# Kernel optimization log

Hardware: AMD Instinct MI355X
Metric: run time of the kernel (lower is better)

## Reference

```python
import jax, jax.numpy as jnp
import numpy as np

B, T, D = 64, 8192, 128

def setup_inputs() -> dict:
    key = jax.random.key(0)
    ks = jax.random.split(key, 6)
    H_r = jax.random.normal(ks[0], (B, T, D), dtype=jnp.float32)
    mask_r = jax.random.randint(ks[1], (B, T), 0, 2, dtype=jnp.int32)
    h_tm1 = jax.random.normal(ks[2], (B, D), dtype=jnp.float32)
    # xavier-ish scaling for linear weights
    s = 1.0 / np.sqrt(D)
    V_w = jax.random.normal(ks[3], (D, D), dtype=jnp.float32) * s
    Wa_w = jax.random.normal(ks[4], (D, D), dtype=jnp.float32) * s
    V_b = jnp.zeros((D,), dtype=jnp.float32)
    Wa_b = jnp.zeros((D,), dtype=jnp.float32)
    v = jax.random.normal(ks[5], (D,), dtype=jnp.float32) * 0.05
    c = jnp.ones((1,), dtype=jnp.float32)
    return {"H_r": H_r, "mask_r": mask_r, "h_tm1": h_tm1, "V_w": V_w,
            "V_b": V_b, "Wa_w": Wa_w, "Wa_b": Wa_b, "v": v, "c": c}

def masked_softmax(x, m, axis=-1):
    x = jnp.clip(x, -15.0, 15.0)
    x = x * m
    e_x = jnp.exp(x - jnp.max(x, axis=axis, keepdims=True))
    e_x = e_x * m
    return e_x / (jnp.sum(e_x, axis=axis, keepdims=True) + 1e-6)

def reference(H_r, mask_r, h_tm1, V_w, V_b, Wa_w, Wa_b, v, c):
    m = mask_r.astype(jnp.float32)                      # [B,T]
    Fk = jnp.einsum('btd,od->bto', H_r, V_w) + V_b      # [B,T,D]
    Fk_prime = h_tm1 @ Wa_w.T + Wa_b                    # [B,D]
    Fk = jnp.tanh(Fk + Fk_prime[:, None, :])
    beta = Fk @ v + c                                   # [B,T]
    beta = masked_softmax(beta, m, axis=-1)
    z = jnp.einsum('bt,btd->bd', beta, H_r)             # [B,D]
    return (z, beta)
```

## Files before the change

### kernel.cpp

```cpp
#include <hip/hip_runtime.h>
#include <math.h>

#define BB 64
#define TT 8192
#define DD 128
#define RPT 64
#define NT 8
#define RPBLK (RPT * NT)
#define NBLK (BB * TT / RPBLK)
#define BPB (TT / RPBLK)

typedef float f32x4 __attribute__((ext_vector_type(4)));
typedef __bf16 bf16x8 __attribute__((ext_vector_type(8)));

__device__ __forceinline__ float fast_tanh(float x) {
    float t = __expf(2.f * x);
    return 1.f - 2.f * __builtin_amdgcn_rcpf(t + 1.f);
}

__device__ __forceinline__ bf16x8 cvt8(f32x4 a, f32x4 b) {
    bf16x8 r;
    r[0] = (__bf16)a[0]; r[1] = (__bf16)a[1]; r[2] = (__bf16)a[2]; r[3] = (__bf16)a[3];
    r[4] = (__bf16)b[0]; r[5] = (__bf16)b[1]; r[6] = (__bf16)b[2]; r[7] = (__bf16)b[3];
    return r;
}

__global__ __launch_bounds__(256) void convw_kernel(const float* __restrict__ Vw,
                                                    __bf16* __restrict__ Vw_bf) {
    const int i = blockIdx.x * 256 + threadIdx.x;
    const int r = i >> 7, cidx = i & 127;
    Vw_bf[r * DD + (cidx ^ ((r & 7) << 3))] = (__bf16)Vw[i];
}

__global__ __launch_bounds__(DD) void fkprime_kernel(
    const float* __restrict__ Waw, const float* __restrict__ Wab,
    const float* __restrict__ h_tm1, float* __restrict__ fkp) {
    const int b = blockIdx.x;
    const int o = threadIdx.x;
    const float* __restrict__ w = Waw + o * DD;
    const float* __restrict__ h = h_tm1 + b * DD;
    float a0 = 0.f, a1 = 0.f, a2 = 0.f, a3 = 0.f;
#pragma unroll
    for (int d = 0; d < DD; d += 4) {
        float4 w4 = *reinterpret_cast<const float4*>(w + d);
        a0 = fmaf(w4.x, h[d + 0], a0);
        a1 = fmaf(w4.y, h[d + 1], a1);
        a2 = fmaf(w4.z, h[d + 2], a2);
        a3 = fmaf(w4.w, h[d + 3], a3);
    }
    fkp[b * DD + o] = (a0 + a1) + (a2 + a3) + Wab[o];
}

__global__ __launch_bounds__(256, 2) void beta_z_kernel(
    const float* __restrict__ H, const __bf16* __restrict__ Vw_bf,
    const float* __restrict__ Vb, const float* __restrict__ fkp,
    const float* __restrict__ vvec, const float* __restrict__ cptr,
    const int* __restrict__ mask,
    float* __restrict__ eout,
    float* __restrict__ zpart) {
    const int tid  = threadIdx.x;
    const int wv   = tid >> 6;
    const int lane = tid & 63;
    const int cl   = lane & 15;
    const int kg   = lane >> 4;
    const int base_row = blockIdx.x * RPBLK;
    const int b    = base_row >> 13;

    __shared__ __align__(16) char s_vw[DD * DD * 2];
    __shared__ __align__(16) char s_h[RPT * DD * 4];
    __shared__ float s_z[4][DD];

    {
        const char* __restrict__ wg = (const char*)Vw_bf;
#pragma unroll
        for (int i = 0; i < 8; ++i) {
            __builtin_amdgcn_global_load_lds(
                (const void*)(wg + wv * 8192 + i * 1024 + lane * 16),
                (void*)(s_vw + wv * 8192 + i * 1024), 16, 0, 0);
        }
    }
    {
        const char* __restrict__ hb =
            (const char*)H + (size_t)(base_row + wv * 16) * 512;
#pragma unroll
        for (int i = 0; i < 8; ++i) {
            const int off  = i * 1024 + lane * 16;
            const int r16  = off >> 9;
            __builtin_amdgcn_global_load_lds(
                (const void*)(hb + (off ^ ((r16 & 7) << 4))),
                (void*)(s_h + wv * 8192 + i * 1024), 16, 0, 0);
        }
    }
    __syncthreads();

    const float cval = cptr[0];
    float biasv[8], vvv[8];
#pragma unroll
    for (int nt = 0; nt < 8; ++nt) {
        const int col = nt * 16 + cl;
        biasv[nt] = Vb[col] + fkp[b * DD + col];
        vvv[nt]   = vvec[col];
    }

    const int ra   = wv * 16 + cl;
    const int swzA = (cl & 7) << 4;
    f32x4 zlo[4], zhi[4];
#pragma unroll
    for (int kk = 0; kk < 4; ++kk) {
        zlo[kk] = (f32x4){0.f, 0.f, 0.f, 0.f};
        zhi[kk] = (f32x4){0.f, 0.f, 0.f, 0.f};
    }

    for (int t = 0; t < NT; ++t) {
        const int grow0 = base_row + t * RPT + wv * 16;
        const float mfl = (float)mask[grow0 + cl];

        f32x4 alo[4], ahi[4];
        bf16x8 af[4];
#pragma unroll
        for (int kk = 0; kk < 4; ++kk) {
            const int abyte = ra * 512 + kk * 128 + kg * 32;
            alo[kk] = *reinterpret_cast<const f32x4*>(s_h + ((abyte)      ^ swzA));
            ahi[kk] = *reinterpret_cast<const f32x4*>(s_h + ((abyte + 16) ^ swzA));
            af[kk]  = cvt8(alo[kk], ahi[kk]);
        }
        __builtin_amdgcn_sched_barrier(0);

        if (t + 1 < NT) {
            const char* __restrict__ hb =
                (const char*)H + (size_t)(grow0 + RPT) * 512;
#pragma unroll
            for (int i = 0; i < 8; ++i) {
                const int off = i * 1024 + lane * 16;
                const int r16 = off >> 9;
                __builtin_amdgcn_global_load_lds(
                    (const void*)(hb + (off ^ ((r16 & 7) << 4))),
                    (void*)(s_h + wv * 8192 + i * 1024), 16, 0, 0);
            }
        }

        f32x4 acc[8];
#pragma unroll
        for (int nt = 0; nt < 8; ++nt) acc[nt] = (f32x4){0.f, 0.f, 0.f, 0.f};
#pragma unroll
        for (int kk = 0; kk < 4; ++kk) {
#pragma unroll
            for (int nt = 0; nt < 8; ++nt) {
                const int rb    = nt * 16 + cl;
                const int bbyte = (rb * 256 + kk * 64 + kg * 16) ^ ((rb & 7) << 4);
                bf16x8 bfr = *reinterpret_cast<const bf16x8*>(s_vw + bbyte);
                acc[nt] = __builtin_amdgcn_mfma_f32_16x16x32_bf16(af[kk], bfr, acc[nt], 0, 0, 0);
            }
        }

        float part[4] = {0.f, 0.f, 0.f, 0.f};
#pragma unroll
        for (int nt = 0; nt < 8; ++nt) {
#pragma unroll
            for (int j = 0; j < 4; ++j)
                part[j] = fmaf(fast_tanh(acc[nt][j] + biasv[nt]), vvv[nt], part[j]);
        }
#pragma unroll
        for (int off = 1; off < 16; off <<= 1) {
#pragma unroll
            for (int j = 0; j < 4; ++j) part[j] += __shfl_xor(part[j], off);
        }
        float epj[4];
#pragma unroll
        for (int j = 0; j < 4; ++j) {
            const float mv = __shfl(mfl, kg * 4 + j);
            const float x  = fminf(fmaxf(cval + part[j], -15.f), 15.f);
            epj[j] = __expf(x * mv - 15.f) * mv;
        }
        if (cl == 0) {
#pragma unroll
            for (int j = 0; j < 4; ++j) eout[grow0 + kg * 4 + j] = epj[j];
        }

        float er0 = __shfl(epj[0], (cl >> 2) << 4);
        float er1 = __shfl(epj[1], (cl >> 2) << 4);
        float er2 = __shfl(epj[2], (cl >> 2) << 4);
        float er3 = __shfl(epj[3], (cl >> 2) << 4);
        const int sel = cl & 3;
        float e_cl = sel == 0 ? er0 : (sel == 1 ? er1 : (sel == 2 ? er2 : er3));
#pragma unroll
        for (int kk = 0; kk < 4; ++kk) {
#pragma unroll
            for (int j = 0; j < 4; ++j) {
                zlo[kk][j] = fmaf(e_cl, alo[kk][j], zlo[kk][j]);
                zhi[kk][j] = fmaf(e_cl, ahi[kk][j], zhi[kk][j]);
            }
        }

        if (t + 1 < NT) asm volatile("s_waitcnt vmcnt(0)" ::: "memory");
    }

#pragma unroll
    for (int off = 1; off < 16; off <<= 1) {
#pragma unroll
        for (int kk = 0; kk < 4; ++kk) {
#pragma unroll
            for (int j = 0; j < 4; ++j) {
                zlo[kk][j] += __shfl_xor(zlo[kk][j], off);
                zhi[kk][j] += __shfl_xor(zhi[kk][j], off);
            }
        }
    }
    if (cl == 0) {
#pragma unroll
        for (int kk = 0; kk < 4; ++kk) {
#pragma unroll
            for (int j = 0; j < 4; ++j) {
                s_z[wv][kk * 32 + kg * 8 + j]     = zlo[kk][j];
                s_z[wv][kk * 32 + kg * 8 + 4 + j] = zhi[kk][j];
            }
        }
    }
    __syncthreads();
    if (tid < DD) {
        zpart[(size_t)blockIdx.x * DD + tid] =
            (s_z[0][tid] + s_z[1][tid]) + (s_z[2][tid] + s_z[3][tid]);
    }
}

__global__ __launch_bounds__(256) void denom_kernel(
    float* __restrict__ eout, const int* __restrict__ mask,
    float* __restrict__ denom) {
    const int b = blockIdx.x, tid = threadIdx.x;
    float* __restrict__ e = eout + (size_t)b * TT;
    const int* __restrict__ mrow = mask + (size_t)b * TT;
    __shared__ float sE[256], sM[256];
    __shared__ int sA[256];

    float E = 0.f, M = 0.f;
    int any0 = 0;
    for (int t = tid; t < TT; t += 256) {
        float ep = e[t];
        E += ep;
        M = fmaxf(M, ep);
        any0 |= (mrow[t] == 0);
    }
    sE[tid] = E; sM[tid] = M; sA[tid] = any0;
    __syncthreads();
    for (int s = 128; s > 0; s >>= 1) {
        if (tid < s) {
            sE[tid] += sE[tid + s];
            sM[tid] = fmaxf(sM[tid], sM[tid + s]);
            sA[tid] |= sA[tid + s];
        }
        __syncthreads();
    }
    const float scale = sA[0] ? fmaxf(sM[0], 3.0590232e-7f ) : sM[0];
    const float dn = sE[0] + 1e-6f * scale;
    if (tid == 0) denom[b] = dn;
    const float inv = 1.f / dn;
    for (int t = tid; t < TT; t += 256) e[t] *= inv;
}

__global__ __launch_bounds__(256) void zfinal_kernel(
    const float* __restrict__ zpart, const float* __restrict__ denom,
    float* __restrict__ out_z) {
    const int idx = blockIdx.x * 256 + threadIdx.x;
    const int b = idx >> 7, d = idx & 127;
    const float* __restrict__ zp = zpart + (size_t)b * BPB * DD + d;
    float s = 0.f;
#pragma unroll
    for (int cc = 0; cc < BPB; ++cc) s += zp[cc * DD];
    out_z[idx] = s / denom[b];
}

extern "C" void kernel_launch(void* const* d_in, const int* in_sizes, int n_in,
                              void* d_out, int out_size, void* d_ws, size_t ws_size,
                              hipStream_t stream) {
    const float* H     = (const float*)d_in[0];
    const int*   mask  = (const int*)d_in[1];
    const float* h_tm1 = (const float*)d_in[2];
    const float* V_w   = (const float*)d_in[3];
    const float* V_b   = (const float*)d_in[4];
    const float* Wa_w  = (const float*)d_in[5];
    const float* Wa_b  = (const float*)d_in[6];
    const float* v     = (const float*)d_in[7];
    const float* c     = (const float*)d_in[8];

    float* out_z    = (float*)d_out;
    float* out_beta = (float*)d_out + BB * DD;

    float* ws     = (float*)d_ws;
    float* fkp    = ws;
    float* zpart  = fkp + BB * DD;
    float* denom  = zpart + NBLK * DD;
    __bf16* Vw_bf = (__bf16*)(denom + BB);

    convw_kernel<<<(DD * DD) / 256, 256, 0, stream>>>(V_w, Vw_bf);
    fkprime_kernel<<<BB, DD, 0, stream>>>(Wa_w, Wa_b, h_tm1, fkp);
    beta_z_kernel<<<NBLK, 256, 0, stream>>>(H, Vw_bf, V_b, fkp, v, c, mask,
                                            out_beta, zpart);
    denom_kernel<<<BB, 256, 0, stream>>>(out_beta, mask, denom);
    zfinal_kernel<<<(BB * DD) / 256, 256, 0, stream>>>(zpart, denom, out_z);
}
```

Baseline: 95.74 us.

## Stage H as bf16 in double-buffered LDS via registers, fuse auxiliary kernels

The main kernel now loads H tiles into registers, converts them to bf16, and writes them into a double-buffered LDS area, replacing direct global-to-LDS fp32 loads and per-iteration conversion. The z accumulation now uses the bf16 copy of H instead of fp32. Rows per block double, which halves the block count. The prep kernels and the denom/zfinal kernels are each fused into one kernel, cutting launches. This trades z precision (bf16 H) and adds a block-wide barrier every iteration plus register staging.

```diff
diff --git a/kernel.cpp b/kernel.cpp
--- a/kernel.cpp
+++ b/kernel.cpp
@@ -5,12 +5,13 @@
 #define TT 8192
 #define DD 128
 #define RPT 64
-#define NT 8
+#define NT 16
 #define RPBLK (RPT * NT)
 #define NBLK (BB * TT / RPBLK)
 #define BPB (TT / RPBLK)
 
 typedef float f32x4 __attribute__((ext_vector_type(4)));
+typedef __bf16 bf16x4 __attribute__((ext_vector_type(4)));
 typedef __bf16 bf16x8 __attribute__((ext_vector_type(8)));
 
 __device__ __forceinline__ float fast_tanh(float x) {
@@ -18,37 +19,32 @@
     return 1.f - 2.f * __builtin_amdgcn_rcpf(t + 1.f);
 }
 
-__device__ __forceinline__ bf16x8 cvt8(f32x4 a, f32x4 b) {
-    bf16x8 r;
-    r[0] = (__bf16)a[0]; r[1] = (__bf16)a[1]; r[2] = (__bf16)a[2]; r[3] = (__bf16)a[3];
-    r[4] = (__bf16)b[0]; r[5] = (__bf16)b[1]; r[6] = (__bf16)b[2]; r[7] = (__bf16)b[3];
-    return r;
-}
-
-__global__ __launch_bounds__(256) void convw_kernel(const float* __restrict__ Vw,
-                                                    __bf16* __restrict__ Vw_bf) {
-    const int i = blockIdx.x * 256 + threadIdx.x;
+__device__ __forceinline__ float bf_at_lo16(unsigned u) { return __uint_as_float(u << 16); }
+__device__ __forceinline__ float bf_at_hi16(unsigned u) { return __uint_as_float(u & 0xffff0000u); }
+
+__global__ __launch_bounds__(256) void prep_kernel(
+    const float* __restrict__ Vw, const float* __restrict__ Waw,
+    const float* __restrict__ Wab, const float* __restrict__ h_tm1,
+    __bf16* __restrict__ Vw_bf, float* __restrict__ fkp) {
+    const int b = blockIdx.x, tid = threadIdx.x;
+    const int i = b * 256 + tid;
     const int r = i >> 7, cidx = i & 127;
     Vw_bf[r * DD + (cidx ^ ((r & 7) << 3))] = (__bf16)Vw[i];
-}
-
-__global__ __launch_bounds__(DD) void fkprime_kernel(
-    const float* __restrict__ Waw, const float* __restrict__ Wab,
-    const float* __restrict__ h_tm1, float* __restrict__ fkp) {
-    const int b = blockIdx.x;
-    const int o = threadIdx.x;
-    const float* __restrict__ w = Waw + o * DD;
-    const float* __restrict__ h = h_tm1 + b * DD;
-    float a0 = 0.f, a1 = 0.f, a2 = 0.f, a3 = 0.f;
-#pragma unroll
-    for (int d = 0; d < DD; d += 4) {
-        float4 w4 = *reinterpret_cast<const float4*>(w + d);
-        a0 = fmaf(w4.x, h[d + 0], a0);
-        a1 = fmaf(w4.y, h[d + 1], a1);
-        a2 = fmaf(w4.z, h[d + 2], a2);
-        a3 = fmaf(w4.w, h[d + 3], a3);
-    }
-    fkp[b * DD + o] = (a0 + a1) + (a2 + a3) + Wab[o];
+
+    if (tid < DD) {
+        const float* __restrict__ w = Waw + tid * DD;
+        const float* __restrict__ h = h_tm1 + b * DD;
+        float a0 = 0.f, a1 = 0.f, a2 = 0.f, a3 = 0.f;
+#pragma unroll
+        for (int d = 0; d < DD; d += 4) {
+            float4 w4 = *reinterpret_cast<const float4*>(w + d);
+            a0 = fmaf(w4.x, h[d + 0], a0);
+            a1 = fmaf(w4.y, h[d + 1], a1);
+            a2 = fmaf(w4.z, h[d + 2], a2);
+            a3 = fmaf(w4.w, h[d + 3], a3);
+        }
+        fkp[b * DD + tid] = (a0 + a1) + (a2 + a3) + Wab[tid];
+    }
 }
 
 __global__ __launch_bounds__(256, 2) void beta_z_kernel(
@@ -67,7 +63,7 @@
     const int b    = base_row >> 13;
 
     __shared__ __align__(16) char s_vw[DD * DD * 2];
-    __shared__ __align__(16) char s_h[RPT * DD * 4];
+    __shared__ __align__(16) char s_h[2][RPT * DD * 2];
     __shared__ float s_z[4][DD];
 
     {
@@ -79,16 +75,20 @@
                 (void*)(s_vw + wv * 8192 + i * 1024), 16, 0, 0);
         }
     }
+    float4 hreg[8];
     {
-        const char* __restrict__ hb =
-            (const char*)H + (size_t)(base_row + wv * 16) * 512;
+        const float4* __restrict__ Hg =
+            reinterpret_cast<const float4*>(H + (size_t)base_row * DD);
+#pragma unroll
+        for (int i = 0; i < 8; ++i) hreg[i] = Hg[i * 256 + tid];
 #pragma unroll
         for (int i = 0; i < 8; ++i) {
-            const int off  = i * 1024 + lane * 16;
-            const int r16  = off >> 9;
-            __builtin_amdgcn_global_load_lds(
-                (const void*)(hb + (off ^ ((r16 & 7) << 4))),
-                (void*)(s_h + wv * 8192 + i * 1024), 16, 0, 0);
+            bf16x4 r;
+            r[0] = (__bf16)hreg[i].x; r[1] = (__bf16)hreg[i].y;
+            r[2] = (__bf16)hreg[i].z; r[3] = (__bf16)hreg[i].w;
+            const int off = (i * 256 + tid) * 8;
+            const int row = off >> 8;
+            *reinterpret_cast<bf16x4*>(s_h[0] + (off ^ ((row & 7) << 4))) = r;
         }
     }
     __syncthreads();
@@ -112,31 +112,25 @@
     }
 
     for (int t = 0; t < NT; ++t) {
-        const int grow0 = base_row + t * RPT + wv * 16;
-        const float mfl = (float)mask[grow0 + cl];
-
-        f32x4 alo[4], ahi[4];
+        const int cur    = t & 1;
+        const int grow0  = base_row + t * RPT;
+        const int myrow0 = grow0 + wv * 16;
+
+        if (t + 1 < NT) {
+            const float4* __restrict__ Hn =
+                reinterpret_cast<const float4*>(H + (size_t)(grow0 + RPT) * DD);
+#pragma unroll
+            for (int i = 0; i < 8; ++i) hreg[i] = Hn[i * 256 + tid];
+        }
+        const float mfl = (float)mask[myrow0 + cl];
+
+        uint4  au[4];
         bf16x8 af[4];
 #pragma unroll
         for (int kk = 0; kk < 4; ++kk) {
-            const int abyte = ra * 512 + kk * 128 + kg * 32;
-            alo[kk] = *reinterpret_cast<const f32x4*>(s_h + ((abyte)      ^ swzA));
-            ahi[kk] = *reinterpret_cast<const f32x4*>(s_h + ((abyte + 16) ^ swzA));
-            af[kk]  = cvt8(alo[kk], ahi[kk]);
-        }
-        __builtin_amdgcn_sched_barrier(0);
-
-        if (t + 1 < NT) {
-            const char* __restrict__ hb =
-                (const char*)H + (size_t)(grow0 + RPT) * 512;
-#pragma unroll
-            for (int i = 0; i < 8; ++i) {
-                const int off = i * 1024 + lane * 16;
-                const int r16 = off >> 9;
-                __builtin_amdgcn_global_load_lds(
-                    (const void*)(hb + (off ^ ((r16 & 7) << 4))),
-                    (void*)(s_h + wv * 8192 + i * 1024), 16, 0, 0);
-            }
+            const int abyte = ra * 256 + kk * 64 + kg * 16;
+            au[kk] = *reinterpret_cast<const uint4*>(s_h[cur] + (abyte ^ swzA));
+            af[kk] = __builtin_bit_cast(bf16x8, au[kk]);
         }
 
         f32x4 acc[8];
@@ -174,25 +168,39 @@
         }
         if (cl == 0) {
 #pragma unroll
-            for (int j = 0; j < 4; ++j) eout[grow0 + kg * 4 + j] = epj[j];
-        }
-
-        float er0 = __shfl(epj[0], (cl >> 2) << 4);
-        float er1 = __shfl(epj[1], (cl >> 2) << 4);
-        float er2 = __shfl(epj[2], (cl >> 2) << 4);
-        float er3 = __shfl(epj[3], (cl >> 2) << 4);
+            for (int j = 0; j < 4; ++j) eout[myrow0 + kg * 4 + j] = epj[j];
+        }
+
+        const float er0 = __shfl(epj[0], (cl >> 2) << 4);
+        const float er1 = __shfl(epj[1], (cl >> 2) << 4);
+        const float er2 = __shfl(epj[2], (cl >> 2) << 4);
+        const float er3 = __shfl(epj[3], (cl >> 2) << 4);
         const int sel = cl & 3;
-        float e_cl = sel == 0 ? er0 : (sel == 1 ? er1 : (sel == 2 ? er2 : er3));
-#pragma unroll
-        for (int kk = 0; kk < 4; ++kk) {
-#pragma unroll
-            for (int j = 0; j < 4; ++j) {
-                zlo[kk][j] = fmaf(e_cl, alo[kk][j], zlo[kk][j]);
-                zhi[kk][j] = fmaf(e_cl, ahi[kk][j], zhi[kk][j]);
+        const float e_cl = sel == 0 ? er0 : (sel == 1 ? er1 : (sel == 2 ? er2 : er3));
+#pragma unroll
+        for (int kk = 0; kk < 4; ++kk) {
+            zlo[kk][0] = fmaf(e_cl, bf_at_lo16(au[kk].x), zlo[kk][0]);
+            zlo[kk][1] = fmaf(e_cl, bf_at_hi16(au[kk].x), zlo[kk][1]);
+            zlo[kk][2] = fmaf(e_cl, bf_at_lo16(au[kk].y), zlo[kk][2]);
+            zlo[kk][3] = fmaf(e_cl, bf_at_hi16(au[kk].y), zlo[kk][3]);
+            zhi[kk][0] = fmaf(e_cl, bf_at_lo16(au[kk].z), zhi[kk][0]);
+            zhi[kk][1] = fmaf(e_cl, bf_at_hi16(au[kk].z), zhi[kk][1]);
+            zhi[kk][2] = fmaf(e_cl, bf_at_lo16(au[kk].w), zhi[kk][2]);
+            zhi[kk][3] = fmaf(e_cl, bf_at_hi16(au[kk].w), zhi[kk][3]);
+        }
+
+        if (t + 1 < NT) {
+#pragma unroll
+            for (int i = 0; i < 8; ++i) {
+                bf16x4 r;
+                r[0] = (__bf16)hreg[i].x; r[1] = (__bf16)hreg[i].y;
+                r[2] = (__bf16)hreg[i].z; r[3] = (__bf16)hreg[i].w;
+                const int off = (i * 256 + tid) * 8;
+                const int row = off >> 8;
+                *reinterpret_cast<bf16x4*>(s_h[cur ^ 1] + (off ^ ((row & 7) << 4))) = r;
             }
         }
-
-        if (t + 1 < NT) asm volatile("s_waitcnt vmcnt(0)" ::: "memory");
+        __syncthreads();
     }
 
 #pragma unroll
@@ -223,9 +231,9 @@
     }
 }
 
-__global__ __launch_bounds__(256) void denom_kernel(
+__global__ __launch_bounds__(256) void denom_z_kernel(
     float* __restrict__ eout, const int* __restrict__ mask,
-    float* __restrict__ denom) {
+    const float* __restrict__ zpart, float* __restrict__ out_z) {
     const int b = blockIdx.x, tid = threadIdx.x;
     float* __restrict__ e = eout + (size_t)b * TT;
     const int* __restrict__ mrow = mask + (size_t)b * TT;
@@ -252,21 +260,17 @@
     }
     const float scale = sA[0] ? fmaxf(sM[0], 3.0590232e-7f ) : sM[0];
     const float dn = sE[0] + 1e-6f * scale;
-    if (tid == 0) denom[b] = dn;
     const float inv = 1.f / dn;
+
     for (int t = tid; t < TT; t += 256) e[t] *= inv;
-}
-
-__global__ __launch_bounds__(256) void zfinal_kernel(
-    const float* __restrict__ zpart, const float* __restrict__ denom,
-    float* __restrict__ out_z) {
-    const int idx = blockIdx.x * 256 + threadIdx.x;
-    const int b = idx >> 7, d = idx & 127;
-    const float* __restrict__ zp = zpart + (size_t)b * BPB * DD + d;
-    float s = 0.f;
-#pragma unroll
-    for (int cc = 0; cc < BPB; ++cc) s += zp[cc * DD];
-    out_z[idx] = s / denom[b];
+
+    if (tid < DD) {
+        const float* __restrict__ zp = zpart + (size_t)b * BPB * DD + tid;
+        float s = 0.f;
+#pragma unroll
+        for (int cc = 0; cc < BPB; ++cc) s += zp[cc * DD];
+        out_z[b * DD + tid] = s * inv;
+    }
 }
 
 extern "C" void kernel_launch(void* const* d_in, const int* in_sizes, int n_in,
@@ -288,13 +292,10 @@
     float* ws     = (float*)d_ws;
     float* fkp    = ws;
     float* zpart  = fkp + BB * DD;
-    float* denom  = zpart + NBLK * DD;
-    __bf16* Vw_bf = (__bf16*)(denom + BB);
-
-    convw_kernel<<<(DD * DD) / 256, 256, 0, stream>>>(V_w, Vw_bf);
-    fkprime_kernel<<<BB, DD, 0, stream>>>(Wa_w, Wa_b, h_tm1, fkp);
+    __bf16* Vw_bf = (__bf16*)(zpart + NBLK * DD);
+
+    prep_kernel<<<BB, 256, 0, stream>>>(V_w, Wa_w, Wa_b, h_tm1, Vw_bf, fkp);
     beta_z_kernel<<<NBLK, 256, 0, stream>>>(H, Vw_bf, V_b, fkp, v, c, mask,
                                             out_beta, zpart);
-    denom_kernel<<<BB, 256, 0, stream>>>(out_beta, mask, denom);
-    zfinal_kernel<<<(BB * DD) / 256, 256, 0, stream>>>(zpart, denom, out_z);
-}
+    denom_z_kernel<<<BB, 256, 0, stream>>>(out_beta, mask, zpart, out_z);
+}
```

Result: faster. 81.04 us (-15.3%).
